# Kernel tuning notes

Measured on AMD Instinct MI355X. Metric: run time of the kernel, lower is better.

## Reference

```python
import jax, jax.numpy as jnp
import numpy as np

D_MODEL = 1024
NUM_HEADS = 16
B, S = 2, 2048


def setup_inputs() -> dict:
    key = jax.random.key(0)
    ks = jax.random.split(key, 11)
    scale = 1.0 / np.sqrt(D_MODEL)
    inp = {
        'q': jax.random.normal(ks[0], (B, S, D_MODEL), jnp.float32),
        'k': jax.random.normal(ks[1], (B, S, D_MODEL), jnp.float32),
        'v': jax.random.normal(ks[2], (B, S, D_MODEL), jnp.float32),
        'w_q': jax.random.normal(ks[3], (D_MODEL, D_MODEL), jnp.float32) * scale,
        'b_q': jax.random.normal(ks[4], (D_MODEL,), jnp.float32) * 0.01,
        'w_k': jax.random.normal(ks[5], (D_MODEL, D_MODEL), jnp.float32) * scale,
        'b_k': jax.random.normal(ks[6], (D_MODEL,), jnp.float32) * 0.01,
        'w_v': jax.random.normal(ks[7], (D_MODEL, D_MODEL), jnp.float32) * scale,
        'b_v': jax.random.normal(ks[8], (D_MODEL,), jnp.float32) * 0.01,
        'w_o': jax.random.normal(ks[9], (D_MODEL, D_MODEL), jnp.float32) * scale,
        'b_o': jax.random.normal(ks[10], (D_MODEL,), jnp.float32) * 0.01,
    }
    return inp


def reference(q, k, v, w_q, b_q, w_k, b_k, w_v, b_v, w_o, b_o):
    Bq, Sq, D = q.shape
    H = NUM_HEADS
    dh = D // H
    # projections (weights stored as [in, out])
    query = q @ w_q + b_q
    key = k @ w_k + b_k
    value = v @ w_v + b_v
    # [B, S, D] -> [B, H, S, dh]
    query = query.reshape(Bq, Sq, H, dh).transpose(0, 2, 1, 3)
    key = key.reshape(Bq, -1, H, dh).transpose(0, 2, 1, 3)
    value = value.reshape(Bq, -1, H, dh).transpose(0, 2, 1, 3)
    # NOTE: original module does NOT scale by 1/sqrt(dh)
    scores = jnp.einsum('bhqd,bhkd->bhqk', query, key)  # [B,H,S,S]
    causal_mask = jnp.triu(jnp.ones((Sq, Sq), dtype=bool), k=1)  # True above diag
    scores = jnp.where(causal_mask[None, None], -jnp.inf, scores)
    attn = jax.nn.softmax(scores, axis=-1)
    data = jnp.einsum('bhqk,bhkd->bhqd', attn, value)  # [B,H,S,dh]
    # FAITHFUL to original bug: transpose(0,1) then view(B, S, -1)
    data = data.transpose(1, 0, 2, 3).reshape(Bq, Sq, -1)  # [H,B,S,dh] -> [B,S,D]
    return data @ w_o + b_o
```

## Files before the change

kernel.cpp:

```cpp
#include <hip/hip_runtime.h>

typedef __fp16 f16;
typedef __fp16 f16x8 __attribute__((ext_vector_type(8)));
typedef __fp16 f16x4 __attribute__((ext_vector_type(4)));
typedef float f32x4 __attribute__((ext_vector_type(4)));

#define D_MODEL 1024
#define SEQ 2048
#define NH 16
#define MTOT 4096

typedef const __attribute__((address_space(1))) unsigned int* gp1_t;
typedef __attribute__((address_space(3))) unsigned int* lp3_t;

__device__ __forceinline__ void gload_lds16(const void* g, void* l) {
  __builtin_amdgcn_global_load_lds((gp1_t)g, (lp3_t)l, 16, 0, 0);
}

__device__ __forceinline__ int permrow(int r) {
  int bp = r >> 11, u = (r >> 7) & 15, t = r & 127;
  int g16 = (bp << 4) | u;
  return ((((g16 & 1) << 4) | (g16 >> 1)) << 7) + t;
}

__global__ __launch_bounds__(256) void cvt_all(const float* __restrict__ q,
                                               const float* __restrict__ k,
                                               const float* __restrict__ v,
                                               const float* __restrict__ wq,
                                               const float* __restrict__ wk,
                                               const float* __restrict__ wv,
                                               const float* __restrict__ wo,
                                               f16* __restrict__ qkv16,
                                               f16* __restrict__ wT) {
  __shared__ float tl[64][65];
  int bid = blockIdx.x, tid = threadIdx.x;
  if (bid < 6144) {
    int i = bid * 256 + tid;
    const int NT = (MTOT * D_MODEL) / 8;
    const float* src;
    int t;
    if (i < NT) { src = q; t = i; }
    else if (i < 2 * NT) { src = k; t = i - NT; }
    else { src = v; t = i - 2 * NT; }
    const float4* s4 = (const float4*)src;
    float4 a = s4[2 * t], b = s4[2 * t + 1];
    f16x8 h;
    h[0] = (f16)a.x; h[1] = (f16)a.y; h[2] = (f16)a.z; h[3] = (f16)a.w;
    h[4] = (f16)b.x; h[5] = (f16)b.y; h[6] = (f16)b.z; h[7] = (f16)b.w;
    *(f16x8*)(qkv16 + (size_t)i * 8) = h;
  } else {
    int bb = bid - 6144;
    int mat = bb >> 8, tile = bb & 255;
    int tk = (tile >> 4) << 6, tn = (tile & 15) << 6;
    const float* W = mat == 0 ? wq : mat == 1 ? wk : mat == 2 ? wv : wo;
    int rr = tid >> 4, c4 = (tid & 15) << 2;
#pragma unroll
    for (int it = 0; it < 4; ++it) {
      const float* p = W + (size_t)(tk + it * 16 + rr) * D_MODEL + tn + c4;
      float4 val = *(const float4*)p;
      tl[it * 16 + rr][c4 + 0] = val.x;
      tl[it * 16 + rr][c4 + 1] = val.y;
      tl[it * 16 + rr][c4 + 2] = val.z;
      tl[it * 16 + rr][c4 + 3] = val.w;
    }
    __syncthreads();
    int n = tid & 63, kseg = (tid >> 6) << 4;
    f16x8 lo, hi;
#pragma unroll
    for (int j = 0; j < 8; ++j) lo[j] = (f16)tl[kseg + j][n];
#pragma unroll
    for (int j = 0; j < 8; ++j) hi[j] = (f16)tl[kseg + 8 + j][n];
    f16* d = wT + (size_t)mat * (D_MODEL * D_MODEL) + (size_t)(tn + n) * D_MODEL + tk + kseg;
    *(f16x8*)d = lo;
    *(f16x8*)(d + 8) = hi;
  }
}

__global__ __launch_bounds__(256, 2) void gemm_qkv(const f16* __restrict__ q16,
                                                   const f16* __restrict__ k16,
                                                   const f16* __restrict__ v16,
                                                   const f16* __restrict__ wT,
                                                   const float* __restrict__ bq,
                                                   const float* __restrict__ bk,
                                                   const float* __restrict__ bv,
                                                   f16* __restrict__ Q16,
                                                   f16* __restrict__ K16,
                                                   f16* __restrict__ VT16) {
  const int K = D_MODEL, N = D_MODEL;
  const size_t WEL = (size_t)D_MODEL * D_MODEL;
  int z = blockIdx.z;
  const f16* A = z == 0 ? q16 : z == 1 ? k16 : v16;
  const f16* BT = wT + (size_t)z * WEL;
  const float* bias = z == 0 ? bq : z == 1 ? bk : bv;

  __shared__ f16 As[128 * 64];
  __shared__ f16 Bs[128 * 64];
  int tid = threadIdx.x;
  int w = tid >> 6, lane = tid & 63;
  int g = lane >> 4, c = lane & 15;
  int wr = w >> 1, wc = w & 1;
  int m0 = blockIdx.x * 128, n0 = blockIdx.y * 128;
  f32x4 acc[4][4] = {};

  for (int kt = 0; kt < K; kt += 64) {
#pragma unroll
    for (int i = 0; i < 4; ++i) {
      int seg = w * 4 + i;
      int p = seg * 1024 + lane * 16;
      int row = p >> 7;
      int colb = (p & 127) ^ ((row & 7) << 4);
      int ae = kt + (colb >> 1);
      gload_lds16(A + (size_t)(m0 + row) * K + ae, &As[seg * 512]);
      gload_lds16(BT + (size_t)(n0 + row) * K + ae, &Bs[seg * 512]);
    }
    __syncthreads();
    f16x8 af[4][2], bf[4][2];
#pragma unroll
    for (int m = 0; m < 4; ++m) {
#pragma unroll
      for (int kk = 0; kk < 2; ++kk) {
        int row = wr * 64 + m * 16 + c;
        int tb = (row * 128 + kk * 64 + g * 16) ^ ((row & 7) << 4);
        af[m][kk] = *(const f16x8*)((const char*)As + tb);
      }
    }
#pragma unroll
    for (int n = 0; n < 4; ++n) {
#pragma unroll
      for (int kk = 0; kk < 2; ++kk) {
        int row = wc * 64 + n * 16 + c;
        int tb = (row * 128 + kk * 64 + g * 16) ^ ((row & 7) << 4);
        bf[n][kk] = *(const f16x8*)((const char*)Bs + tb);
      }
    }
    __builtin_amdgcn_s_setprio(1);
#pragma unroll
    for (int m = 0; m < 4; ++m)
#pragma unroll
      for (int n = 0; n < 4; ++n)
#pragma unroll
        for (int kk = 0; kk < 2; ++kk)
          acc[m][n] = __builtin_amdgcn_mfma_f32_16x16x32_f16(af[m][kk], bf[n][kk], acc[m][n], 0, 0, 0);
    __builtin_amdgcn_s_setprio(0);
    __syncthreads();
  }

  int rb = m0 + wr * 64;
  int cb = n0 + wc * 64;
  if (z < 2) {
    f16* O = z == 0 ? Q16 : K16;
#pragma unroll
    for (int m = 0; m < 4; ++m) {
      int row0 = rb + m * 16 + 4 * g;
#pragma unroll
      for (int n = 0; n < 4; ++n) {
        int col = cb + n * 16 + c;
        float bv2 = bias[col];
#pragma unroll
        for (int r = 0; r < 4; ++r) O[(size_t)(row0 + r) * N + col] = (f16)(acc[m][n][r] + bv2);
      }
    }
  } else {
    f16* O = VT16;
#pragma unroll
    for (int m = 0; m < 4; ++m) {
      int s0f = rb + m * 16 + 4 * g;
      int bb = s0f >> 11, s = s0f & (SEQ - 1);
#pragma unroll
      for (int n = 0; n < 4; ++n) {
        int col = cb + n * 16 + c;
        float bv2 = bias[col];
        f16x4 hv;
#pragma unroll
        for (int r = 0; r < 4; ++r) hv[r] = (f16)(acc[m][n][r] + bv2);
        *(f16x4*)(O + ((size_t)(bb * NH + (col >> 6)) * 64 + (col & 63)) * SEQ + s) = hv;
      }
    }
  }
}

__global__ __launch_bounds__(256, 2) void gemm_out(const f16* __restrict__ A,
                                                   const f16* __restrict__ BT,
                                                   const float* __restrict__ bias,
                                                   float* __restrict__ O) {
  const int K = D_MODEL, N = D_MODEL;
  __shared__ f16 As[64 * 64];
  __shared__ f16 Bs[128 * 64];
  int tid = threadIdx.x;
  int w = tid >> 6, lane = tid & 63;
  int g = lane >> 4, c = lane & 15;
  int wr = w >> 1, wc = w & 1;
  int m0 = blockIdx.x * 64, n0 = blockIdx.y * 128;
  f32x4 acc[2][4] = {};

  for (int kt = 0; kt < K; kt += 64) {
#pragma unroll
    for (int i = 0; i < 2; ++i) {
      int seg = w * 2 + i;
      int p = seg * 1024 + lane * 16;
      int row = p >> 7;
      int colb = (p & 127) ^ ((row & 7) << 4);
      int ae = kt + (colb >> 1);
      gload_lds16(A + (size_t)permrow(m0 + row) * K + ae, &As[seg * 512]);
    }
#pragma unroll
    for (int i = 0; i < 4; ++i) {
      int seg = w * 4 + i;
      int p = seg * 1024 + lane * 16;
      int row = p >> 7;
      int colb = (p & 127) ^ ((row & 7) << 4);
      int ae = kt + (colb >> 1);
      gload_lds16(BT + (size_t)(n0 + row) * K + ae, &Bs[seg * 512]);
    }
    __syncthreads();
    f16x8 af[2][2], bf[4][2];
#pragma unroll
    for (int m = 0; m < 2; ++m) {
#pragma unroll
      for (int kk = 0; kk < 2; ++kk) {
        int row = wr * 32 + m * 16 + c;
        int tb = (row * 128 + kk * 64 + g * 16) ^ ((row & 7) << 4);
        af[m][kk] = *(const f16x8*)((const char*)As + tb);
      }
    }
#pragma unroll
    for (int n = 0; n < 4; ++n) {
#pragma unroll
      for (int kk = 0; kk < 2; ++kk) {
        int row = wc * 64 + n * 16 + c;
        int tb = (row * 128 + kk * 64 + g * 16) ^ ((row & 7) << 4);
        bf[n][kk] = *(const f16x8*)((const char*)Bs + tb);
      }
    }
    __builtin_amdgcn_s_setprio(1);
#pragma unroll
    for (int m = 0; m < 2; ++m)
#pragma unroll
      for (int n = 0; n < 4; ++n)
#pragma unroll
        for (int kk = 0; kk < 2; ++kk)
          acc[m][n] = __builtin_amdgcn_mfma_f32_16x16x32_f16(af[m][kk], bf[n][kk], acc[m][n], 0, 0, 0);
    __builtin_amdgcn_s_setprio(0);
    __syncthreads();
  }

  int rb = m0 + wr * 32;
  int cb = n0 + wc * 64;
#pragma unroll
  for (int m = 0; m < 2; ++m) {
    int row0 = rb + m * 16 + 4 * g;
#pragma unroll
    for (int n = 0; n < 4; ++n) {
      int col = cb + n * 16 + c;
      float bv = bias[col];
#pragma unroll
      for (int r = 0; r < 4; ++r) O[(size_t)(row0 + r) * N + col] = acc[m][n][r] + bv;
    }
  }
}

#define THR2 11.5f
__global__ __launch_bounds__(256, 2) void attn_kernel(const f16* __restrict__ Q,
                                                      const f16* __restrict__ K,
                                                      const f16* __restrict__ VT,
                                                      f16* __restrict__ AO) {
  __shared__ f16 Ksh[2][64 * 64];
  __shared__ f16 Vsh[2][64 * 64];
  __shared__ f16 Psh[4][16 * 64];
  int tid = threadIdx.x;
  int w = tid >> 6, lane = tid & 63;
  int g = lane >> 4, c = lane & 15;
  int blk = blockIdx.x;
  int bh = blk & 31;
  int uu = blk >> 5;
  int grp = uu & 7, pos = uu >> 3;
  int cb = pos == 0 ? grp : pos == 1 ? 15 - grp : pos == 2 ? 16 + grp : 31 - grp;
  int b = bh >> 4, h = bh & 15;
  int q0 = cb * 64 + w * 16;
  const int NT = cb + 1;
  const size_t brow = (size_t)b * SEQ;
  const int hcol = h * 64;

  int srow = w * 8 + (lane >> 3);
  int seo = (((lane & 7) ^ (srow & 7)) << 3);
  const f16* Kg0 = K + (size_t)(brow + srow) * D_MODEL + hcol + seo;
  const f16* Kg1 = K + (size_t)(brow + srow + 32) * D_MODEL + hcol + seo;
  const f16* Vg0 = VT + ((size_t)bh * 64 + srow) * SEQ + seo;
  const f16* Vg1 = VT + ((size_t)bh * 64 + srow + 32) * SEQ + seo;

  char* Pw = (char*)&Psh[w][0];
  const f16 LOG2E = (f16)1.44269504f;

  f16x8 qf[2];
#pragma unroll
  for (int kk = 0; kk < 2; ++kk) {
    qf[kk] = *(const f16x8*)(Q + (size_t)(brow + q0 + c) * D_MODEL + hcol + kk * 32 + 8 * g);
#pragma unroll
    for (int j = 0; j < 8; ++j) qf[kk][j] = (f16)(qf[kk][j] * LOG2E);
  }

  float m_st[4], l_st[4];
  f32x4 o[4] = {};
#pragma unroll
  for (int r = 0; r < 4; ++r) { m_st[r] = -1e30f; l_st[r] = 0.f; }

  gload_lds16(Kg0, &Ksh[0][w * 512]);
  gload_lds16(Kg1, &Ksh[0][2048 + w * 512]);
  gload_lds16(Vg0, &Vsh[0][w * 512]);
  gload_lds16(Vg1, &Vsh[0][2048 + w * 512]);
  __syncthreads();

  int cur = 0;
  for (int t = 0; t < NT; ++t) {
    if (t + 1 < NT) {
      int kv1 = (t + 1) * 64;
      int nx = cur ^ 1;
      gload_lds16(Kg0 + (size_t)kv1 * D_MODEL, &Ksh[nx][w * 512]);
      gload_lds16(Kg1 + (size_t)kv1 * D_MODEL, &Ksh[nx][2048 + w * 512]);
      gload_lds16(Vg0 + kv1, &Vsh[nx][w * 512]);
      gload_lds16(Vg1 + kv1, &Vsh[nx][2048 + w * 512]);
    }
    {
      int kv0 = t * 64;
      const char* Kb = (const char*)&Ksh[cur][0];
      const char* Vb = (const char*)&Vsh[cur][0];
      f16x8 kf[4][2];
#pragma unroll
      for (int n = 0; n < 4; ++n) {
        int row = n * 16 + c;
#pragma unroll
        for (int kk = 0; kk < 2; ++kk)
          kf[n][kk] = *(const f16x8*)(Kb + ((row * 128 + kk * 64 + g * 16) ^ ((row & 7) << 4)));
      }
      f32x4 s[4] = {};
      __builtin_amdgcn_s_setprio(1);
#pragma unroll
      for (int n = 0; n < 4; ++n)
#pragma unroll
        for (int kk = 0; kk < 2; ++kk)
          s[n] = __builtin_amdgcn_mfma_f32_16x16x32_f16(qf[kk], kf[n][kk], s[n], 0, 0, 0);
      __builtin_amdgcn_s_setprio(0);
      if (t == NT - 1) {
#pragma unroll
        for (int n = 0; n < 4; ++n) {
          int kv = kv0 + n * 16 + c;
#pragma unroll
          for (int r = 0; r < 4; ++r)
            if (kv > q0 + 4 * g + r) s[n][r] = -1e30f;
        }
      }
      float pmax[4];
      int flag = 0;
#pragma unroll
      for (int r = 0; r < 4; ++r) {
        pmax[r] = fmaxf(fmaxf(s[0][r], s[1][r]), fmaxf(s[2][r], s[3][r]));
        flag |= (pmax[r] > m_st[r] + THR2) ? 1 : 0;
      }
      if (__any(flag)) {
#pragma unroll
        for (int r = 0; r < 4; ++r) {
          float mx = pmax[r];
          mx = fmaxf(mx, __shfl_xor(mx, 1));
          mx = fmaxf(mx, __shfl_xor(mx, 2));
          mx = fmaxf(mx, __shfl_xor(mx, 4));
          mx = fmaxf(mx, __shfl_xor(mx, 8));
          float mnew = fmaxf(m_st[r], mx);
          float corr = __builtin_amdgcn_exp2f(m_st[r] - mnew);
          l_st[r] *= corr;
#pragma unroll
          for (int nd = 0; nd < 4; ++nd) o[nd][r] *= corr;
          m_st[r] = mnew;
        }
      }
#pragma unroll
      for (int r = 0; r < 4; ++r) {
#pragma unroll
        for (int n = 0; n < 4; ++n) {
          float pv = __builtin_amdgcn_exp2f(s[n][r] - m_st[r]);
          s[n][r] = pv;
          l_st[r] += pv;
        }
      }
#pragma unroll
      for (int n = 0; n < 4; ++n)
#pragma unroll
        for (int r = 0; r < 4; ++r) {
          int prow = 4 * g + r;
          *(f16*)(Pw + ((prow * 128 + (n * 16 + c) * 2) ^ ((prow & 7) << 4))) = (f16)s[n][r];
        }
      f16x8 vf[4][2];
#pragma unroll
      for (int nd = 0; nd < 4; ++nd) {
        int row = nd * 16 + c;
#pragma unroll
        for (int kb = 0; kb < 2; ++kb)
          vf[nd][kb] = *(const f16x8*)(Vb + ((row * 128 + kb * 64 + g * 16) ^ ((row & 7) << 4)));
      }
      f16x8 pa[2];
#pragma unroll
      for (int kb = 0; kb < 2; ++kb)
        pa[kb] = *(const f16x8*)(Pw + ((c * 128 + kb * 64 + g * 16) ^ ((c & 7) << 4)));
      __builtin_amdgcn_s_setprio(1);
#pragma unroll
      for (int nd = 0; nd < 4; ++nd)
#pragma unroll
        for (int kb = 0; kb < 2; ++kb)
          o[nd] = __builtin_amdgcn_mfma_f32_16x16x32_f16(pa[kb], vf[nd][kb], o[nd], 0, 0, 0);
      __builtin_amdgcn_s_setprio(0);
    }
    __syncthreads();
    cur ^= 1;
  }

#pragma unroll
  for (int r = 0; r < 4; ++r) {
    float l = l_st[r];
    l += __shfl_xor(l, 1);
    l += __shfl_xor(l, 2);
    l += __shfl_xor(l, 4);
    l += __shfl_xor(l, 8);
    l_st[r] = 1.0f / l;
  }
#pragma unroll
  for (int nd = 0; nd < 4; ++nd) {
#pragma unroll
    for (int r = 0; r < 4; ++r) {
      float val = o[nd][r] * l_st[r];
      AO[((size_t)bh * SEQ + q0 + 4 * g + r) * 64 + nd * 16 + c] = (f16)val;
    }
  }
}

extern "C" void kernel_launch(void* const* d_in, const int* in_sizes, int n_in,
                              void* d_out, int out_size, void* d_ws, size_t ws_size,
                              hipStream_t stream) {
  const float* q  = (const float*)d_in[0];
  const float* k  = (const float*)d_in[1];
  const float* v  = (const float*)d_in[2];
  const float* wq = (const float*)d_in[3];
  const float* bq = (const float*)d_in[4];
  const float* wk = (const float*)d_in[5];
  const float* bk = (const float*)d_in[6];
  const float* wv = (const float*)d_in[7];
  const float* bv = (const float*)d_in[8];
  const float* wo = (const float*)d_in[9];
  const float* bo = (const float*)d_in[10];

  const size_t TEN = (size_t)MTOT * D_MODEL;
  const size_t WEL = (size_t)D_MODEL * D_MODEL;
  f16* ws  = (f16*)d_ws;
  f16* q16 = ws;
  f16* k16 = q16 + TEN;
  f16* v16 = k16 + TEN;
  f16* wT  = v16 + TEN;
  f16* Q16 = wT + 4 * WEL;
  f16* K16 = Q16 + TEN;
  f16* VT16 = K16 + TEN;
  f16* AO  = q16;

  cvt_all<<<7168, 256, 0, stream>>>(q, k, v, wq, wk, wv, wo, q16, wT);
  gemm_qkv<<<dim3(32, 8, 3), 256, 0, stream>>>(q16, k16, v16, wT, bq, bk, bv, Q16, K16, VT16);
  attn_kernel<<<1024, 256, 0, stream>>>(Q16, K16, VT16, AO);
  gemm_out<<<dim3(64, 8), 256, 0, stream>>>(AO, wT + 3 * WEL, bo, (float*)d_out);
}
```

Before: 123.4 us.

## Rewrite attention with 32x32x16 MFMA, transposed scores, in-register P via permlane32 swap

The attention kernel now runs 2 waves of 32 query rows each instead of 4 waves of 16, using 32x32x16 f16 MFMAs. It computes S^T = K·Q^T so each lane owns one query column, which turns the row max and sum into a single cross-half shuffle. P is packed to f16 with cvt_pkrtz and rearranged with v_permlane32_swap instead of a round trip through LDS. The aim is to remove the P shared-memory traffic and shuffle reductions and to raise MFMA efficiency, at the cost of fewer waves per block, more registers per lane, and round-toward-zero conversion of P.

```diff
diff --git a/kernel.cpp b/kernel.cpp
--- a/kernel.cpp
+++ b/kernel.cpp
@@ -3,7 +3,9 @@
 typedef __fp16 f16;
 typedef __fp16 f16x8 __attribute__((ext_vector_type(8)));
 typedef __fp16 f16x4 __attribute__((ext_vector_type(4)));
+typedef __fp16 f16x2 __attribute__((ext_vector_type(2)));
 typedef float f32x4 __attribute__((ext_vector_type(4)));
+typedef float f32x16 __attribute__((ext_vector_type(16)));
 
 #define D_MODEL 1024
 #define SEQ 2048
@@ -21,6 +23,12 @@
   int bp = r >> 11, u = (r >> 7) & 15, t = r & 127;
   int g16 = (bp << 4) | u;
   return ((((g16 & 1) << 4) | (g16 >> 1)) << 7) + t;
+}
+
+__device__ __forceinline__ unsigned int pkrtz(float a, float b) {
+  union { f16x2 h; unsigned int u; } z;
+  z.h = __builtin_amdgcn_cvt_pkrtz(a, b);
+  return z.u;
 }
 
 __global__ __launch_bounds__(256) void cvt_all(const float* __restrict__ q,
@@ -260,174 +268,164 @@
 }
 
 #define THR2 11.5f
-__global__ __launch_bounds__(256, 2) void attn_kernel(const f16* __restrict__ Q,
+__global__ __launch_bounds__(128, 2) void attn_kernel(const f16* __restrict__ Q,
                                                       const f16* __restrict__ K,
                                                       const f16* __restrict__ VT,
                                                       f16* __restrict__ AO) {
-  __shared__ f16 Ksh[2][64 * 64];
-  __shared__ f16 Vsh[2][64 * 64];
-  __shared__ f16 Psh[4][16 * 64];
+  __shared__ __attribute__((aligned(16))) f16 Ksh[2][64 * 64];
+  __shared__ __attribute__((aligned(16))) f16 Vsh[2][64 * 64];
   int tid = threadIdx.x;
   int w = tid >> 6, lane = tid & 63;
-  int g = lane >> 4, c = lane & 15;
+  int c = lane & 31, hi = lane >> 5;
   int blk = blockIdx.x;
   int bh = blk & 31;
   int uu = blk >> 5;
   int grp = uu & 7, pos = uu >> 3;
   int cb = pos == 0 ? grp : pos == 1 ? 15 - grp : pos == 2 ? 16 + grp : 31 - grp;
   int b = bh >> 4, h = bh & 15;
-  int q0 = cb * 64 + w * 16;
+  int q0 = cb * 64 + w * 32;
   const int NT = cb + 1;
   const size_t brow = (size_t)b * SEQ;
   const int hcol = h * 64;
 
-  int srow = w * 8 + (lane >> 3);
-  int seo = (((lane & 7) ^ (srow & 7)) << 3);
-  const f16* Kg0 = K + (size_t)(brow + srow) * D_MODEL + hcol + seo;
-  const f16* Kg1 = K + (size_t)(brow + srow + 32) * D_MODEL + hcol + seo;
-  const f16* Vg0 = VT + ((size_t)bh * 64 + srow) * SEQ + seo;
-  const f16* Vg1 = VT + ((size_t)bh * 64 + srow + 32) * SEQ + seo;
-
-  char* Pw = (char*)&Psh[w][0];
+  int sr = lane >> 3;
+  int seo = ((lane & 7) ^ sr) << 3;
+  const f16* Kgb = K + (size_t)(brow + w * 32 + sr) * D_MODEL + hcol + seo;
+  const f16* Vgb = VT + ((size_t)bh * 64 + w * 32 + sr) * SEQ + seo;
+
   const f16 LOG2E = (f16)1.44269504f;
-
-  f16x8 qf[2];
-#pragma unroll
-  for (int kk = 0; kk < 2; ++kk) {
-    qf[kk] = *(const f16x8*)(Q + (size_t)(brow + q0 + c) * D_MODEL + hcol + kk * 32 + 8 * g);
+  f16x8 qf[4];
+  const f16* Qp = Q + (size_t)(brow + q0 + c) * D_MODEL + hcol + 8 * hi;
+#pragma unroll
+  for (int kk = 0; kk < 4; ++kk) {
+    qf[kk] = *(const f16x8*)(Qp + 16 * kk);
 #pragma unroll
     for (int j = 0; j < 8; ++j) qf[kk][j] = (f16)(qf[kk][j] * LOG2E);
   }
 
-  float m_st[4], l_st[4];
-  f32x4 o[4] = {};
-#pragma unroll
-  for (int r = 0; r < 4; ++r) { m_st[r] = -1e30f; l_st[r] = 0.f; }
-
-  gload_lds16(Kg0, &Ksh[0][w * 512]);
-  gload_lds16(Kg1, &Ksh[0][2048 + w * 512]);
-  gload_lds16(Vg0, &Vsh[0][w * 512]);
-  gload_lds16(Vg1, &Vsh[0][2048 + w * 512]);
+  float m_st = -1e30f, l_st = 0.f;
+  f32x16 o0 = {}, o1 = {};
+
+#pragma unroll
+  for (int j = 0; j < 4; ++j) {
+    gload_lds16(Kgb + (size_t)(j * 8) * D_MODEL, &Ksh[0][(w * 32 + j * 8) * 64]);
+    gload_lds16(Vgb + (size_t)(j * 8) * SEQ, &Vsh[0][(w * 32 + j * 8) * 64]);
+  }
   __syncthreads();
 
+  int rsw = (c & 7) << 4;
   int cur = 0;
   for (int t = 0; t < NT; ++t) {
     if (t + 1 < NT) {
       int kv1 = (t + 1) * 64;
       int nx = cur ^ 1;
-      gload_lds16(Kg0 + (size_t)kv1 * D_MODEL, &Ksh[nx][w * 512]);
-      gload_lds16(Kg1 + (size_t)kv1 * D_MODEL, &Ksh[nx][2048 + w * 512]);
-      gload_lds16(Vg0 + kv1, &Vsh[nx][w * 512]);
-      gload_lds16(Vg1 + kv1, &Vsh[nx][2048 + w * 512]);
-    }
-    {
-      int kv0 = t * 64;
-      const char* Kb = (const char*)&Ksh[cur][0];
-      const char* Vb = (const char*)&Vsh[cur][0];
-      f16x8 kf[4][2];
-#pragma unroll
-      for (int n = 0; n < 4; ++n) {
-        int row = n * 16 + c;
-#pragma unroll
-        for (int kk = 0; kk < 2; ++kk)
-          kf[n][kk] = *(const f16x8*)(Kb + ((row * 128 + kk * 64 + g * 16) ^ ((row & 7) << 4)));
-      }
-      f32x4 s[4] = {};
-      __builtin_amdgcn_s_setprio(1);
-#pragma unroll
-      for (int n = 0; n < 4; ++n)
-#pragma unroll
-        for (int kk = 0; kk < 2; ++kk)
-          s[n] = __builtin_amdgcn_mfma_f32_16x16x32_f16(qf[kk], kf[n][kk], s[n], 0, 0, 0);
-      __builtin_amdgcn_s_setprio(0);
-      if (t == NT - 1) {
-#pragma unroll
-        for (int n = 0; n < 4; ++n) {
-          int kv = kv0 + n * 16 + c;
-#pragma unroll
-          for (int r = 0; r < 4; ++r)
-            if (kv > q0 + 4 * g + r) s[n][r] = -1e30f;
-        }
-      }
-      float pmax[4];
-      int flag = 0;
-#pragma unroll
-      for (int r = 0; r < 4; ++r) {
-        pmax[r] = fmaxf(fmaxf(s[0][r], s[1][r]), fmaxf(s[2][r], s[3][r]));
-        flag |= (pmax[r] > m_st[r] + THR2) ? 1 : 0;
-      }
-      if (__any(flag)) {
-#pragma unroll
-        for (int r = 0; r < 4; ++r) {
-          float mx = pmax[r];
-          mx = fmaxf(mx, __shfl_xor(mx, 1));
-          mx = fmaxf(mx, __shfl_xor(mx, 2));
-          mx = fmaxf(mx, __shfl_xor(mx, 4));
-          mx = fmaxf(mx, __shfl_xor(mx, 8));
-          float mnew = fmaxf(m_st[r], mx);
-          float corr = __builtin_amdgcn_exp2f(m_st[r] - mnew);
-          l_st[r] *= corr;
-#pragma unroll
-          for (int nd = 0; nd < 4; ++nd) o[nd][r] *= corr;
-          m_st[r] = mnew;
-        }
-      }
-#pragma unroll
-      for (int r = 0; r < 4; ++r) {
-#pragma unroll
-        for (int n = 0; n < 4; ++n) {
-          float pv = __builtin_amdgcn_exp2f(s[n][r] - m_st[r]);
-          s[n][r] = pv;
-          l_st[r] += pv;
-        }
-      }
-#pragma unroll
-      for (int n = 0; n < 4; ++n)
-#pragma unroll
-        for (int r = 0; r < 4; ++r) {
-          int prow = 4 * g + r;
-          *(f16*)(Pw + ((prow * 128 + (n * 16 + c) * 2) ^ ((prow & 7) << 4))) = (f16)s[n][r];
-        }
-      f16x8 vf[4][2];
-#pragma unroll
-      for (int nd = 0; nd < 4; ++nd) {
-        int row = nd * 16 + c;
-#pragma unroll
-        for (int kb = 0; kb < 2; ++kb)
-          vf[nd][kb] = *(const f16x8*)(Vb + ((row * 128 + kb * 64 + g * 16) ^ ((row & 7) << 4)));
-      }
-      f16x8 pa[2];
-#pragma unroll
-      for (int kb = 0; kb < 2; ++kb)
-        pa[kb] = *(const f16x8*)(Pw + ((c * 128 + kb * 64 + g * 16) ^ ((c & 7) << 4)));
-      __builtin_amdgcn_s_setprio(1);
-#pragma unroll
-      for (int nd = 0; nd < 4; ++nd)
-#pragma unroll
-        for (int kb = 0; kb < 2; ++kb)
-          o[nd] = __builtin_amdgcn_mfma_f32_16x16x32_f16(pa[kb], vf[nd][kb], o[nd], 0, 0, 0);
-      __builtin_amdgcn_s_setprio(0);
-    }
+#pragma unroll
+      for (int j = 0; j < 4; ++j) {
+        gload_lds16(Kgb + (size_t)(kv1 + j * 8) * D_MODEL, &Ksh[nx][(w * 32 + j * 8) * 64]);
+        gload_lds16(Vgb + (size_t)(j * 8) * SEQ + kv1, &Vsh[nx][(w * 32 + j * 8) * 64]);
+      }
+    }
+    const char* Kb = (const char*)&Ksh[cur][0];
+    const char* Vb = (const char*)&Vsh[cur][0];
+    f16x8 kf[2][4];
+#pragma unroll
+    for (int ks = 0; ks < 2; ++ks)
+#pragma unroll
+      for (int kk = 0; kk < 4; ++kk)
+        kf[ks][kk] = *(const f16x8*)(Kb + (((ks * 32 + c) * 128 + 32 * kk + 16 * hi) ^ rsw));
+    f32x16 s0 = {}, s1 = {};
+    __builtin_amdgcn_s_setprio(1);
+#pragma unroll
+    for (int kk = 0; kk < 4; ++kk) {
+      s0 = __builtin_amdgcn_mfma_f32_32x32x16_f16(kf[0][kk], qf[kk], s0, 0, 0, 0);
+      s1 = __builtin_amdgcn_mfma_f32_32x32x16_f16(kf[1][kk], qf[kk], s1, 0, 0, 0);
+    }
+    __builtin_amdgcn_s_setprio(0);
+    if (t == NT - 1) {
+      int q = q0 + c;
+      int kvb = t * 64 + 4 * hi;
+#pragma unroll
+      for (int r = 0; r < 16; ++r) {
+        int kv = kvb + (r & 3) + 8 * (r >> 2);
+        if (kv > q) s0[r] = -1e30f;
+        if (kv + 32 > q) s1[r] = -1e30f;
+      }
+    }
+    float t8[8];
+#pragma unroll
+    for (int r = 0; r < 8; ++r)
+      t8[r] = fmaxf(fmaxf(s0[r], s0[r + 8]), fmaxf(s1[r], s1[r + 8]));
+    float pm = fmaxf(fmaxf(fmaxf(t8[0], t8[1]), fmaxf(t8[2], t8[3])),
+                     fmaxf(fmaxf(t8[4], t8[5]), fmaxf(t8[6], t8[7])));
+    float mx = fmaxf(pm, __shfl_xor(pm, 32));
+    if (__any(mx > m_st + THR2)) {
+      float mnew = fmaxf(m_st, mx);
+      float corr = __builtin_amdgcn_exp2f(m_st - mnew);
+      l_st *= corr;
+#pragma unroll
+      for (int r = 0; r < 16; ++r) { o0[r] *= corr; o1[r] *= corr; }
+      m_st = mnew;
+    }
+    float lacc = 0.f;
+#pragma unroll
+    for (int r = 0; r < 16; ++r) {
+      float p0 = __builtin_amdgcn_exp2f(s0[r] - m_st);
+      float p1 = __builtin_amdgcn_exp2f(s1[r] - m_st);
+      s0[r] = p0; s1[r] = p1;
+      lacc += p0 + p1;
+    }
+    l_st += lacc;
+    union PU { unsigned int u[4]; f16x8 v; };
+    PU pu[4];
+#pragma unroll
+    for (int kk = 0; kk < 4; ++kk) {
+      int rb = 8 * (kk & 1);
+      unsigned int la0, la1, lb0, lb1;
+      if (kk < 2) {
+        la0 = pkrtz(s0[rb + 0], s0[rb + 1]);
+        la1 = pkrtz(s0[rb + 2], s0[rb + 3]);
+        lb0 = pkrtz(s0[rb + 4], s0[rb + 5]);
+        lb1 = pkrtz(s0[rb + 6], s0[rb + 7]);
+      } else {
+        la0 = pkrtz(s1[rb + 0], s1[rb + 1]);
+        la1 = pkrtz(s1[rb + 2], s1[rb + 3]);
+        lb0 = pkrtz(s1[rb + 4], s1[rb + 5]);
+        lb1 = pkrtz(s1[rb + 6], s1[rb + 7]);
+      }
+      asm("v_permlane32_swap_b32 %0, %1" : "+v"(la0), "+v"(lb0));
+      asm("v_permlane32_swap_b32 %0, %1" : "+v"(la1), "+v"(lb1));
+      pu[kk].u[0] = la0; pu[kk].u[1] = la1; pu[kk].u[2] = lb0; pu[kk].u[3] = lb1;
+    }
+    f16x8 vf[2][4];
+#pragma unroll
+    for (int dt = 0; dt < 2; ++dt)
+#pragma unroll
+      for (int kk = 0; kk < 4; ++kk)
+        vf[dt][kk] = *(const f16x8*)(Vb + (((dt * 32 + c) * 128 + 32 * kk + 16 * hi) ^ rsw));
+    __builtin_amdgcn_s_setprio(1);
+#pragma unroll
+    for (int kk = 0; kk < 4; ++kk) {
+      o0 = __builtin_amdgcn_mfma_f32_32x32x16_f16(vf[0][kk], pu[kk].v, o0, 0, 0, 0);
+      o1 = __builtin_amdgcn_mfma_f32_32x32x16_f16(vf[1][kk], pu[kk].v, o1, 0, 0, 0);
+    }
+    __builtin_amdgcn_s_setprio(0);
     __syncthreads();
     cur ^= 1;
   }
 
-#pragma unroll
-  for (int r = 0; r < 4; ++r) {
-    float l = l_st[r];
-    l += __shfl_xor(l, 1);
-    l += __shfl_xor(l, 2);
-    l += __shfl_xor(l, 4);
-    l += __shfl_xor(l, 8);
-    l_st[r] = 1.0f / l;
-  }
-#pragma unroll
-  for (int nd = 0; nd < 4; ++nd) {
+  float lt = l_st + __shfl_xor(l_st, 32);
+  float linv = 1.0f / lt;
+  f16* aoq = AO + ((size_t)bh * SEQ + q0 + c) * 64 + 4 * hi;
+#pragma unroll
+  for (int rq = 0; rq < 4; ++rq) {
+    f16x4 h0, h1;
 #pragma unroll
     for (int r = 0; r < 4; ++r) {
-      float val = o[nd][r] * l_st[r];
-      AO[((size_t)bh * SEQ + q0 + 4 * g + r) * 64 + nd * 16 + c] = (f16)val;
-    }
+      h0[r] = (f16)(o0[4 * rq + r] * linv);
+      h1[r] = (f16)(o1[4 * rq + r] * linv);
+    }
+    *(f16x4*)(aoq + 8 * rq) = h0;
+    *(f16x4*)(aoq + 32 + 8 * rq) = h1;
   }
 }
 
@@ -460,6 +458,6 @@
 
   cvt_all<<<7168, 256, 0, stream>>>(q, k, v, wq, wk, wv, wo, q16, wT);
   gemm_qkv<<<dim3(32, 8, 3), 256, 0, stream>>>(q16, k16, v16, wT, bq, bk, bv, Q16, K16, VT16);
-  attn_kernel<<<1024, 256, 0, stream>>>(Q16, K16, VT16, AO);
+  attn_kernel<<<1024, 128, 0, stream>>>(Q16, K16, VT16, AO);
   gemm_out<<<dim3(64, 8), 256, 0, stream>>>(AO, wT + 3 * WEL, bo, (float*)d_out);
 }
```

Measured after the change: 122.6 us. About the same (-0.6%).
